# Optimization experiments

Hardware: AMD Instinct MI355X
Metric: run time of the kernel (lower is better)

The kernel has to match this reference:

```python
import jax, jax.numpy as jnp
import numpy as np

DIM = 768
NUM_HEADS = 12
HEAD_DIM = DIM // NUM_HEADS
SCALE = HEAD_DIM ** -0.5


def setup_inputs() -> dict:
    key = jax.random.key(0)
    k_x, k_qw, k_qb, k_pw, k_pb = jax.random.split(key, 5)
    B, N = 4, 2048
    x = jax.random.normal(k_x, (B, N, DIM), dtype=jnp.float32)
    s = 1.0 / np.sqrt(DIM)
    qkv_w = jax.random.normal(k_qw, (3 * DIM, DIM), dtype=jnp.float32) * s
    qkv_b = jax.random.normal(k_qb, (3 * DIM,), dtype=jnp.float32) * 0.02
    proj_w = jax.random.normal(k_pw, (DIM, DIM), dtype=jnp.float32) * s
    proj_b = jax.random.normal(k_pb, (DIM,), dtype=jnp.float32) * 0.02
    return {"x": x, "qkv_w": qkv_w, "qkv_b": qkv_b, "proj_w": proj_w, "proj_b": proj_b}


def reference(x, qkv_w, qkv_b, proj_w, proj_b):
    B, N, D = x.shape
    H, Hd = NUM_HEADS, HEAD_DIM
    # qkv linear: [B,N,3D] -> [3,B,H,N,Hd]
    qkv = (x @ qkv_w.T + qkv_b).reshape(B, N, 3, H, Hd).transpose(2, 0, 3, 1, 4)
    q, k, v = qkv[0], qkv[1], qkv[2]
    scores = jnp.einsum("bhnd,bhmd->bhnm", q, k) * SCALE  # [B,H,N,N]
    attn = jax.nn.softmax(scores, axis=-1)
    out = jnp.einsum("bhnm,bhmd->bhnd", attn, v)  # [B,H,N,Hd]
    out = out.transpose(0, 2, 1, 3).reshape(B, N, D)
    return out @ proj_w.T + proj_b
```

## Files before the change

### kernel.cpp

```cpp
#include <hip/hip_runtime.h>

#define SEQ 2048
#define NB 4
#define NH 12
#define DHEAD 64
#define DMODEL 768
#define D3 2304
#define MTOT 8192
#define QSCALE 0.18033688011112042f

typedef float f4v __attribute__((ext_vector_type(4)));
typedef float fl4 __attribute__((ext_vector_type(4)));
typedef short s8v __attribute__((ext_vector_type(8)));
typedef __bf16 b8v __attribute__((ext_vector_type(8)));
typedef unsigned int ui4 __attribute__((ext_vector_type(4)));
typedef unsigned int ui2 __attribute__((ext_vector_type(2)));
typedef unsigned short us4 __attribute__((ext_vector_type(4)));

#define GLDS16(g, l)                                                            \
  __builtin_amdgcn_global_load_lds(                                             \
      (const __attribute__((address_space(1))) void*)(g),                       \
      (__attribute__((address_space(3))) void*)(l), 16, 0, 0)

__device__ inline float fast_exp2(float x) {
#if __has_builtin(__builtin_amdgcn_exp2f)
  return __builtin_amdgcn_exp2f(x);
#else
  float r;
  asm("v_exp_f32 %0, %1" : "=v"(r) : "v"(x));
  return r;
#endif
}

template <typename T>
__device__ inline auto mfma_try(T a, T b, f4v c, int)
    -> decltype(__builtin_amdgcn_mfma_f32_16x16x32_bf16(a, b, c, 0, 0, 0)) {
  return __builtin_amdgcn_mfma_f32_16x16x32_bf16(a, b, c, 0, 0, 0);
}
template <typename T>
__device__ inline f4v mfma_try(T a, T b, f4v c, long) {
  return __builtin_amdgcn_mfma_f32_16x16x32_bf16(
      __builtin_bit_cast(b8v, a), __builtin_bit_cast(b8v, b), c, 0, 0, 0);
}
__device__ inline f4v mfma16(s8v a, s8v b, f4v c) { return mfma_try(a, b, c, 0); }

__device__ inline unsigned short f2bf(float f) {
  union { float f; unsigned u; } v; v.f = f;
  unsigned r = v.u + 0x7FFFu + ((v.u >> 16) & 1u);
  return (unsigned short)(r >> 16);
}

__device__ inline unsigned pack2(float a, float b) {
  unsigned ua = __builtin_bit_cast(unsigned, a) + 0x8000u;
  unsigned ub = __builtin_bit_cast(unsigned, b) + 0x8000u;
  return __builtin_amdgcn_perm(ub, ua, 0x07060302u);
}

#define NX4 1572864
#define NW14 442368
#define NW24 147456
__global__ void k_cvt(const float* __restrict__ x, const float* __restrict__ w1,
                      const float* __restrict__ w2, unsigned short* __restrict__ ox,
                      unsigned short* __restrict__ o1, unsigned short* __restrict__ o2) {
  int i = blockIdx.x * 256 + threadIdx.x;
  const float* src;
  unsigned short* dst;
  int off;
  if (i < NX4) { src = x; dst = ox; off = i; }
  else if (i < NX4 + NW14) { src = w1; dst = o1; off = i - NX4; }
  else if (i < NX4 + NW14 + NW24) { src = w2; dst = o2; off = i - NX4 - NW14; }
  else return;
  fl4 f = ((const fl4*)src)[off];
  us4 o;
  o[0] = f2bf(f[0]); o[1] = f2bf(f[1]); o[2] = f2bf(f[2]); o[3] = f2bf(f[3]);
  ((us4*)dst)[off] = o;
}

template <int EPI>
__global__ __launch_bounds__(256, 3) void k_gemm_nt(
    const unsigned short* __restrict__ A,
    const unsigned short* __restrict__ Bm,
    const float* __restrict__ bias,
    float* __restrict__ outF,
    unsigned short* __restrict__ outQ,
    unsigned short* __restrict__ outK,
    unsigned short* __restrict__ outV,
    int K) {
  __shared__ unsigned short As[128 * 64];
  __shared__ unsigned short Bs[128 * 64];
  const int tid = threadIdx.x;
  const int lane = tid & 63;
  const int wave = tid >> 6;
  const int wr = wave >> 1, wc = wave & 1;
  const int lr = lane & 15;
  const int lq = lane >> 4;
  const int rowBase = blockIdx.y * 128;
  const int colBase = blockIdx.x * 128;

  f4v acc[4][4];
#pragma unroll
  for (int i = 0; i < 4; ++i)
#pragma unroll
    for (int j = 0; j < 4; ++j) acc[i][j] = f4v{0.f, 0.f, 0.f, 0.f};

  const int srow = wave * 8 + (lane >> 3);
  const int scol = ((lane & 7) ^ ((lane >> 3) & 7)) * 8;
  const unsigned short* Ag0 = A + (long)(rowBase + srow) * K + scol;
  const unsigned short* Bg0 = Bm + (long)(colBase + srow) * K + scol;
  unsigned short* Al0 = &As[srow * 64 + (lane & 7) * 8];
  unsigned short* Bl0 = &Bs[srow * 64 + (lane & 7) * 8];
  const int kTiles = K >> 6;
  const int swz = (lr & 7);

  for (int kt = 0; kt < kTiles; ++kt) {
#pragma unroll
    for (int p = 0; p < 4; ++p) {
      GLDS16(Ag0 + kt * 64 + p * 32 * K, Al0 + p * 32 * 64);
      GLDS16(Bg0 + kt * 64 + p * 32 * K, Bl0 + p * 32 * 64);
    }
    __syncthreads();
#pragma unroll
    for (int ks = 0; ks < 2; ++ks) {
      s8v af[4], bf[4];
#pragma unroll
      for (int i = 0; i < 4; ++i)
        af[i] = *(const s8v*)&As[(wr * 64 + i * 16 + lr) * 64 + ((ks * 4 + lq) ^ swz) * 8];
#pragma unroll
      for (int j = 0; j < 4; ++j)
        bf[j] = *(const s8v*)&Bs[(wc * 64 + j * 16 + lr) * 64 + ((ks * 4 + lq) ^ swz) * 8];
#pragma unroll
      for (int i = 0; i < 4; ++i)
#pragma unroll
        for (int j = 0; j < 4; ++j) acc[i][j] = mfma16(af[i], bf[j], acc[i][j]);
    }
    __syncthreads();
  }

  if (EPI == 0 || EPI == 1) {
    const int fw = rowBase + wr * 64;
    fl4 bv[4];
#pragma unroll
    for (int i = 0; i < 4; ++i) bv[i] = *(const fl4*)&bias[fw + i * 16 + lq * 4];
    const int isQ = (EPI == 0) && (fw < DMODEL);
    const int h = (fw >> 6) % NH;
    const unsigned short* outQK = isQ ? outQ : outK;
    const float scl = isQ ? QSCALE : 1.0f;
#pragma unroll
    for (int j = 0; j < 4; ++j) {
      const int ng = colBase + wc * 64 + j * 16 + lr;
#pragma unroll
      for (int i = 0; i < 4; ++i) {
        float v0 = acc[i][j][0] + bv[i][0], v1 = acc[i][j][1] + bv[i][1];
        float v2 = acc[i][j][2] + bv[i][2], v3 = acc[i][j][3] + bv[i][3];
        if (EPI == 1) {
          *(fl4*)&outF[(long)ng * DMODEL + fw + i * 16 + lq * 4] = fl4{v0, v1, v2, v3};
        } else {
          const int b = ng >> 11, nn = ng & 2047;
          unsigned short* dst = (unsigned short*)outQK +
              (long)(((b * NH + h) * SEQ) + nn) * DHEAD + (i * 16 + lq * 4);
          *(ui2*)dst = ui2{pack2(v0 * scl, v1 * scl), pack2(v2 * scl, v3 * scl)};
        }
      }
    }
  } else {
#pragma unroll
    for (int j = 0; j < 4; ++j) {
      const int col = colBase + wc * 64 + j * 16 + lr;
      const float bvs = bias[col];
      const int h = col >> 6, hd = col & 63;
#pragma unroll
      for (int i = 0; i < 4; ++i) {
        const int row = rowBase + wr * 64 + i * 16 + lq * 4;
        const int b = row >> 11, n = row & 2047;
        const int bq = (n >> 2) & 7;
        const int np = (n & ~31) + ((bq & 3) << 3) + ((bq >> 2) << 2);
        float v0 = acc[i][j][0] + bvs, v1 = acc[i][j][1] + bvs;
        float v2 = acc[i][j][2] + bvs, v3 = acc[i][j][3] + bvs;
        *(ui2*)&outV[(long)(((b * NH + h) * DHEAD) + hd) * SEQ + np] =
            ui2{pack2(v0, v1), pack2(v2, v3)};
      }
    }
  }
}

__global__ __launch_bounds__(256, 3) void k_attn(
    const unsigned short* __restrict__ Q,
    const unsigned short* __restrict__ Kg,
    const unsigned short* __restrict__ Vt,
    unsigned short* __restrict__ Ob) {
  __shared__ unsigned short Ks[128 * 64];
  __shared__ unsigned short Vs[64 * 128];
  const int tid = threadIdx.x;
  const int lane = tid & 63;
  const int wave = tid >> 6;
  const int lr = lane & 15;
  const int lq = lane >> 4;
  const int bh = blockIdx.y;
  const int b = bh / NH, h = bh % NH;
  const int q0 = blockIdx.x * 128;
  const unsigned short* Qb = Q + (long)bh * SEQ * DHEAD;
  const unsigned short* Kb = Kg + (long)bh * SEQ * DHEAD;
  const unsigned short* Vb = Vt + (long)bh * DHEAD * SEQ;

  s8v qf[2][2];
#pragma unroll
  for (int i = 0; i < 2; ++i)
#pragma unroll
    for (int ss = 0; ss < 2; ++ss)
      qf[i][ss] = *(const s8v*)(Qb + (q0 + wave * 32 + i * 16 + lr) * DHEAD + ss * 32 + lq * 8);

  f4v o[2][4];
  f4v la[2] = {f4v{0.f, 0.f, 0.f, 0.f}, f4v{0.f, 0.f, 0.f, 0.f}};
  const f4v zc = f4v{0.f, 0.f, 0.f, 0.f};
  const s8v ones = {0x3F80, 0x3F80, 0x3F80, 0x3F80, 0x3F80, 0x3F80, 0x3F80, 0x3F80};
#pragma unroll
  for (int i = 0; i < 2; ++i)
#pragma unroll
    for (int jo = 0; jo < 4; ++jo) o[i][jo] = f4v{0.f, 0.f, 0.f, 0.f};

  const int srow = wave * 8 + (lane >> 3);
  const int scol = ((lane & 7) ^ ((lane >> 3) & 7)) * 8;
  const unsigned short* Kg0 = Kb + (long)srow * DHEAD + scol;
  unsigned short* Kl0 = &Ks[srow * 64 + (lane & 7) * 8];
  const int swz = (lr & 7);
  const int vdrow = wave * 4 + (lane >> 4);
  const int vchunk = (lane & 15) ^ vdrow;
  const unsigned short* Vg0 = Vb + (long)vdrow * SEQ + vchunk * 8;
  unsigned short* Vl0 = &Vs[vdrow * 128 + (lane & 15) * 8];

  for (int kt = 0; kt < SEQ / 128; ++kt) {
#pragma unroll
    for (int p = 0; p < 4; ++p)
      GLDS16(Kg0 + (long)(kt * 128 + p * 32) * DHEAD, Kl0 + p * 32 * 64);
#pragma unroll
    for (int p = 0; p < 4; ++p)
      GLDS16(Vg0 + (long)(p * 16) * SEQ + kt * 128, Vl0 + p * 16 * 128);
    __syncthreads();

    f4v s[2][8];
#pragma unroll
    for (int t = 0; t < 8; ++t) {
      s8v kf0 = *(const s8v*)&Ks[(t * 16 + lr) * 64 + ((0 * 4 + lq) ^ swz) * 8];
      s8v kf1 = *(const s8v*)&Ks[(t * 16 + lr) * 64 + ((1 * 4 + lq) ^ swz) * 8];
      s[0][t] = mfma16(kf0, qf[0][0], zc);
      s[1][t] = mfma16(kf0, qf[1][0], zc);
      s[0][t] = mfma16(kf1, qf[0][1], s[0][t]);
      s[1][t] = mfma16(kf1, qf[1][1], s[1][t]);
    }

    unsigned pk[2][8][2];
#pragma unroll
    for (int i = 0; i < 2; ++i)
#pragma unroll
      for (int t = 0; t < 8; ++t) {
        float p0 = fast_exp2(s[i][t][0]);
        float p1 = fast_exp2(s[i][t][1]);
        float p2 = fast_exp2(s[i][t][2]);
        float p3 = fast_exp2(s[i][t][3]);
        pk[i][t][0] = pack2(p0, p1);
        pk[i][t][1] = pack2(p2, p3);
      }

#pragma unroll
    for (int ss = 0; ss < 4; ++ss) {
      s8v vf[4];
#pragma unroll
      for (int jo = 0; jo < 4; ++jo)
        vf[jo] = *(const s8v*)&Vs[(jo * 16 + lr) * 128 + ((ss * 4 + lq) ^ lr) * 8];
#pragma unroll
      for (int i = 0; i < 2; ++i) {
        s8v pf = __builtin_bit_cast(
            s8v, ui4{pk[i][2 * ss][0], pk[i][2 * ss][1], pk[i][2 * ss + 1][0], pk[i][2 * ss + 1][1]});
        la[i] = mfma16(ones, pf, la[i]);
#pragma unroll
        for (int jo = 0; jo < 4; ++jo) o[i][jo] = mfma16(vf[jo], pf, o[i][jo]);
      }
    }
    __syncthreads();
  }

  float linv[2];
  linv[0] = 1.0f / la[0][0];
  linv[1] = 1.0f / la[1][0];

#pragma unroll
  for (int i = 0; i < 2; ++i) {
    const long nrow = (long)(b * SEQ + q0 + wave * 32 + i * 16 + lr) * DMODEL;
#pragma unroll
    for (int jo = 0; jo < 4; ++jo) {
      float v0 = o[i][jo][0] * linv[i];
      float v1 = o[i][jo][1] * linv[i];
      float v2 = o[i][jo][2] * linv[i];
      float v3 = o[i][jo][3] * linv[i];
      *(ui2*)(Ob + nrow + h * DHEAD + jo * 16 + lq * 4) = ui2{pack2(v0, v1), pack2(v2, v3)};
    }
  }
}

extern "C" void kernel_launch(void* const* d_in, const int* in_sizes, int n_in,
                              void* d_out, int out_size, void* d_ws, size_t ws_size,
                              hipStream_t stream) {
  (void)in_sizes; (void)n_in; (void)out_size; (void)ws_size;
  const float* x = (const float*)d_in[0];
  const float* qkv_w = (const float*)d_in[1];
  const float* qkv_b = (const float*)d_in[2];
  const float* proj_w = (const float*)d_in[3];
  const float* proj_b = (const float*)d_in[4];
  float* out = (float*)d_out;

  unsigned short* ws = (unsigned short*)d_ws;
  unsigned short* xb = ws;
  unsigned short* wqkvb = xb + 6291456;
  unsigned short* wprjb = wqkvb + 1769472;
  unsigned short* qb = wprjb + 589824;
  unsigned short* kb = qb + 6291456;
  unsigned short* vtb = kb + 6291456;
  unsigned short* aob = vtb + 6291456;

  k_cvt<<<(NX4 + NW14 + NW24 + 255) / 256, 256, 0, stream>>>(
      x, qkv_w, proj_w, xb, wqkvb, wprjb);

  k_gemm_nt<0><<<dim3(MTOT / 128, 2 * DMODEL / 128), 256, 0, stream>>>(
      wqkvb, xb, qkv_b, nullptr, qb, kb, nullptr, DMODEL);
  k_gemm_nt<2><<<dim3(DMODEL / 128, MTOT / 128), 256, 0, stream>>>(
      xb, wqkvb + 2 * DMODEL * DMODEL, qkv_b + 2 * DMODEL, nullptr, nullptr, nullptr, vtb,
      DMODEL);
  k_attn<<<dim3(SEQ / 128, NB * NH), 256, 0, stream>>>(qb, kb, vtb, aob);
  k_gemm_nt<1><<<dim3(MTOT / 128, DMODEL / 128), 256, 0, stream>>>(
      wprjb, aob, proj_b, out, nullptr, nullptr, nullptr, DMODEL);
}
```

Baseline: 207.1 us.

## Merge Q/K and V GEMMs into one launch and shrink tiles for V and proj

Q/K and V projection GEMMs are fused into a single launch, where block index selects either a 128x128 Q/K tile or a 128x64 V tile. The V and output-projection GEMMs now use 128x64 tiles, so they launch more blocks. This is meant to remove one kernel launch gap and improve wave fill for the smaller GEMMs. In exchange, the narrower tiles reuse less data from shared memory per block.

```diff
diff --git a/kernel.cpp b/kernel.cpp
--- a/kernel.cpp
+++ b/kernel.cpp
@@ -76,97 +76,128 @@
   ((us4*)dst)[off] = o;
 }
 
-template <int EPI>
-__global__ __launch_bounds__(256, 3) void k_gemm_nt(
-    const unsigned short* __restrict__ A,
-    const unsigned short* __restrict__ Bm,
-    const float* __restrict__ bias,
-    float* __restrict__ outF,
+__global__ __launch_bounds__(256, 3) void k_qkv(
+    const unsigned short* __restrict__ xb,
+    const unsigned short* __restrict__ wb,
+    const float* __restrict__ qkv_b,
     unsigned short* __restrict__ outQ,
     unsigned short* __restrict__ outK,
-    unsigned short* __restrict__ outV,
-    int K) {
+    unsigned short* __restrict__ outV) {
   __shared__ unsigned short As[128 * 64];
   __shared__ unsigned short Bs[128 * 64];
   const int tid = threadIdx.x;
   const int lane = tid & 63;
   const int wave = tid >> 6;
   const int wr = wave >> 1, wc = wave & 1;
-  const int lr = lane & 15;
-  const int lq = lane >> 4;
-  const int rowBase = blockIdx.y * 128;
-  const int colBase = blockIdx.x * 128;
-
-  f4v acc[4][4];
-#pragma unroll
-  for (int i = 0; i < 4; ++i)
-#pragma unroll
-    for (int j = 0; j < 4; ++j) acc[i][j] = f4v{0.f, 0.f, 0.f, 0.f};
-
+  const int lr = lane & 15, lq = lane >> 4;
   const int srow = wave * 8 + (lane >> 3);
   const int scol = ((lane & 7) ^ ((lane >> 3) & 7)) * 8;
-  const unsigned short* Ag0 = A + (long)(rowBase + srow) * K + scol;
-  const unsigned short* Bg0 = Bm + (long)(colBase + srow) * K + scol;
-  unsigned short* Al0 = &As[srow * 64 + (lane & 7) * 8];
-  unsigned short* Bl0 = &Bs[srow * 64 + (lane & 7) * 8];
-  const int kTiles = K >> 6;
   const int swz = (lr & 7);
-
-  for (int kt = 0; kt < kTiles; ++kt) {
-#pragma unroll
-    for (int p = 0; p < 4; ++p) {
-      GLDS16(Ag0 + kt * 64 + p * 32 * K, Al0 + p * 32 * 64);
-      GLDS16(Bg0 + kt * 64 + p * 32 * K, Bl0 + p * 32 * 64);
-    }
-    __syncthreads();
-#pragma unroll
-    for (int ks = 0; ks < 2; ++ks) {
-      s8v af[4], bf[4];
-#pragma unroll
-      for (int i = 0; i < 4; ++i)
-        af[i] = *(const s8v*)&As[(wr * 64 + i * 16 + lr) * 64 + ((ks * 4 + lq) ^ swz) * 8];
-#pragma unroll
-      for (int j = 0; j < 4; ++j)
-        bf[j] = *(const s8v*)&Bs[(wc * 64 + j * 16 + lr) * 64 + ((ks * 4 + lq) ^ swz) * 8];
-#pragma unroll
-      for (int i = 0; i < 4; ++i)
-#pragma unroll
-        for (int j = 0; j < 4; ++j) acc[i][j] = mfma16(af[i], bf[j], acc[i][j]);
-    }
-    __syncthreads();
-  }
-
-  if (EPI == 0 || EPI == 1) {
+  const int bx = blockIdx.x;
+
+  if (bx < 768) {
+    const int rowBase = (bx >> 6) * 128;
+    const int colBase = (bx & 63) * 128;
+    f4v acc[4][4];
+#pragma unroll
+    for (int i = 0; i < 4; ++i)
+#pragma unroll
+      for (int j = 0; j < 4; ++j) acc[i][j] = f4v{0.f, 0.f, 0.f, 0.f};
+
+    const unsigned short* Ag0 = wb + (long)(rowBase + srow) * DMODEL + scol;
+    const unsigned short* Bg0 = xb + (long)(colBase + srow) * DMODEL + scol;
+    unsigned short* Al0 = &As[srow * 64 + (lane & 7) * 8];
+    unsigned short* Bl0 = &Bs[srow * 64 + (lane & 7) * 8];
+
+    for (int kt = 0; kt < DMODEL / 64; ++kt) {
+#pragma unroll
+      for (int p = 0; p < 4; ++p) {
+        GLDS16(Ag0 + kt * 64 + p * 32 * DMODEL, Al0 + p * 32 * 64);
+        GLDS16(Bg0 + kt * 64 + p * 32 * DMODEL, Bl0 + p * 32 * 64);
+      }
+      __syncthreads();
+#pragma unroll
+      for (int ks = 0; ks < 2; ++ks) {
+        s8v af[4], bf[4];
+#pragma unroll
+        for (int i = 0; i < 4; ++i)
+          af[i] = *(const s8v*)&As[(wr * 64 + i * 16 + lr) * 64 + ((ks * 4 + lq) ^ swz) * 8];
+#pragma unroll
+        for (int j = 0; j < 4; ++j)
+          bf[j] = *(const s8v*)&Bs[(wc * 64 + j * 16 + lr) * 64 + ((ks * 4 + lq) ^ swz) * 8];
+#pragma unroll
+        for (int i = 0; i < 4; ++i)
+#pragma unroll
+          for (int j = 0; j < 4; ++j) acc[i][j] = mfma16(af[i], bf[j], acc[i][j]);
+      }
+      __syncthreads();
+    }
+
     const int fw = rowBase + wr * 64;
     fl4 bv[4];
 #pragma unroll
-    for (int i = 0; i < 4; ++i) bv[i] = *(const fl4*)&bias[fw + i * 16 + lq * 4];
-    const int isQ = (EPI == 0) && (fw < DMODEL);
+    for (int i = 0; i < 4; ++i) bv[i] = *(const fl4*)&qkv_b[fw + i * 16 + lq * 4];
+    const int isQ = fw < DMODEL;
     const int h = (fw >> 6) % NH;
-    const unsigned short* outQK = isQ ? outQ : outK;
+    unsigned short* outQK = (unsigned short*)(isQ ? outQ : outK);
     const float scl = isQ ? QSCALE : 1.0f;
 #pragma unroll
     for (int j = 0; j < 4; ++j) {
       const int ng = colBase + wc * 64 + j * 16 + lr;
+      const int b = ng >> 11, nn = ng & 2047;
 #pragma unroll
       for (int i = 0; i < 4; ++i) {
-        float v0 = acc[i][j][0] + bv[i][0], v1 = acc[i][j][1] + bv[i][1];
-        float v2 = acc[i][j][2] + bv[i][2], v3 = acc[i][j][3] + bv[i][3];
-        if (EPI == 1) {
-          *(fl4*)&outF[(long)ng * DMODEL + fw + i * 16 + lq * 4] = fl4{v0, v1, v2, v3};
-        } else {
-          const int b = ng >> 11, nn = ng & 2047;
-          unsigned short* dst = (unsigned short*)outQK +
-              (long)(((b * NH + h) * SEQ) + nn) * DHEAD + (i * 16 + lq * 4);
-          *(ui2*)dst = ui2{pack2(v0 * scl, v1 * scl), pack2(v2 * scl, v3 * scl)};
-        }
+        float v0 = (acc[i][j][0] + bv[i][0]) * scl, v1 = (acc[i][j][1] + bv[i][1]) * scl;
+        float v2 = (acc[i][j][2] + bv[i][2]) * scl, v3 = (acc[i][j][3] + bv[i][3]) * scl;
+        *(ui2*)(outQK + (long)(((b * NH + h) * SEQ) + nn) * DHEAD + (i * 16 + lq * 4)) =
+            ui2{pack2(v0, v1), pack2(v2, v3)};
       }
     }
   } else {
-#pragma unroll
-    for (int j = 0; j < 4; ++j) {
-      const int col = colBase + wc * 64 + j * 16 + lr;
-      const float bvs = bias[col];
+    const int vb = bx - 768;
+    const int rowBase = (vb / 12) * 128;
+    const int colBase = (vb % 12) * 64;
+    f4v acc[4][2];
+#pragma unroll
+    for (int i = 0; i < 4; ++i)
+#pragma unroll
+      for (int j = 0; j < 2; ++j) acc[i][j] = f4v{0.f, 0.f, 0.f, 0.f};
+
+    const unsigned short* Ag0 = xb + (long)(rowBase + srow) * DMODEL + scol;
+    const unsigned short* Bg0 =
+        wb + (long)(2 * DMODEL + colBase + srow) * DMODEL + scol;
+    unsigned short* Al0 = &As[srow * 64 + (lane & 7) * 8];
+    unsigned short* Bl0 = &Bs[srow * 64 + (lane & 7) * 8];
+
+    for (int kt = 0; kt < DMODEL / 64; ++kt) {
+#pragma unroll
+      for (int p = 0; p < 4; ++p)
+        GLDS16(Ag0 + kt * 64 + p * 32 * DMODEL, Al0 + p * 32 * 64);
+#pragma unroll
+      for (int p = 0; p < 2; ++p)
+        GLDS16(Bg0 + kt * 64 + p * 32 * DMODEL, Bl0 + p * 32 * 64);
+      __syncthreads();
+#pragma unroll
+      for (int ks = 0; ks < 2; ++ks) {
+        s8v af[4], bf[2];
+#pragma unroll
+        for (int i = 0; i < 4; ++i)
+          af[i] = *(const s8v*)&As[(wr * 64 + i * 16 + lr) * 64 + ((ks * 4 + lq) ^ swz) * 8];
+#pragma unroll
+        for (int j = 0; j < 2; ++j)
+          bf[j] = *(const s8v*)&Bs[(wc * 32 + j * 16 + lr) * 64 + ((ks * 4 + lq) ^ swz) * 8];
+#pragma unroll
+        for (int i = 0; i < 4; ++i)
+#pragma unroll
+          for (int j = 0; j < 2; ++j) acc[i][j] = mfma16(af[i], bf[j], acc[i][j]);
+      }
+      __syncthreads();
+    }
+
+#pragma unroll
+    for (int j = 0; j < 2; ++j) {
+      const int col = colBase + wc * 32 + j * 16 + lr;
+      const float bvs = qkv_b[2 * DMODEL + col];
       const int h = col >> 6, hd = col & 63;
 #pragma unroll
       for (int i = 0; i < 4; ++i) {
@@ -179,6 +210,76 @@
         *(ui2*)&outV[(long)(((b * NH + h) * DHEAD) + hd) * SEQ + np] =
             ui2{pack2(v0, v1), pack2(v2, v3)};
       }
+    }
+  }
+}
+
+__global__ __launch_bounds__(256, 3) void k_proj(
+    const unsigned short* __restrict__ Wp,
+    const unsigned short* __restrict__ Xt,
+    const float* __restrict__ bias,
+    float* __restrict__ outF) {
+  __shared__ unsigned short As[128 * 64];
+  __shared__ unsigned short Bs[64 * 64];
+  const int tid = threadIdx.x;
+  const int lane = tid & 63;
+  const int wave = tid >> 6;
+  const int wr = wave >> 1, wc = wave & 1;
+  const int lr = lane & 15, lq = lane >> 4;
+  const int srow = wave * 8 + (lane >> 3);
+  const int scol = ((lane & 7) ^ ((lane >> 3) & 7)) * 8;
+  const int swz = (lr & 7);
+  const int rowBase = blockIdx.y * 128;
+  const int colBase = blockIdx.x * 64;
+
+  f4v acc[4][2];
+#pragma unroll
+  for (int i = 0; i < 4; ++i)
+#pragma unroll
+    for (int j = 0; j < 2; ++j) acc[i][j] = f4v{0.f, 0.f, 0.f, 0.f};
+
+  const unsigned short* Ag0 = Wp + (long)(rowBase + srow) * DMODEL + scol;
+  const unsigned short* Bg0 = Xt + (long)(colBase + srow) * DMODEL + scol;
+  unsigned short* Al0 = &As[srow * 64 + (lane & 7) * 8];
+  unsigned short* Bl0 = &Bs[srow * 64 + (lane & 7) * 8];
+
+  for (int kt = 0; kt < DMODEL / 64; ++kt) {
+#pragma unroll
+    for (int p = 0; p < 4; ++p)
+      GLDS16(Ag0 + kt * 64 + p * 32 * DMODEL, Al0 + p * 32 * 64);
+#pragma unroll
+    for (int p = 0; p < 2; ++p)
+      GLDS16(Bg0 + kt * 64 + p * 32 * DMODEL, Bl0 + p * 32 * 64);
+    __syncthreads();
+#pragma unroll
+    for (int ks = 0; ks < 2; ++ks) {
+      s8v af[4], bf[2];
+#pragma unroll
+      for (int i = 0; i < 4; ++i)
+        af[i] = *(const s8v*)&As[(wr * 64 + i * 16 + lr) * 64 + ((ks * 4 + lq) ^ swz) * 8];
+#pragma unroll
+      for (int j = 0; j < 2; ++j)
+        bf[j] = *(const s8v*)&Bs[(wc * 32 + j * 16 + lr) * 64 + ((ks * 4 + lq) ^ swz) * 8];
+#pragma unroll
+      for (int i = 0; i < 4; ++i)
+#pragma unroll
+        for (int j = 0; j < 2; ++j) acc[i][j] = mfma16(af[i], bf[j], acc[i][j]);
+    }
+    __syncthreads();
+  }
+
+  const int fw = rowBase + wr * 64;
+  fl4 bv[4];
+#pragma unroll
+  for (int i = 0; i < 4; ++i) bv[i] = *(const fl4*)&bias[fw + i * 16 + lq * 4];
+#pragma unroll
+  for (int j = 0; j < 2; ++j) {
+    const int ng = colBase + wc * 32 + j * 16 + lr;
+#pragma unroll
+    for (int i = 0; i < 4; ++i) {
+      float v0 = acc[i][j][0] + bv[i][0], v1 = acc[i][j][1] + bv[i][1];
+      float v2 = acc[i][j][2] + bv[i][2], v3 = acc[i][j][3] + bv[i][3];
+      *(fl4*)&outF[(long)ng * DMODEL + fw + i * 16 + lq * 4] = fl4{v0, v1, v2, v3};
     }
   }
 }
@@ -320,12 +421,7 @@
   k_cvt<<<(NX4 + NW14 + NW24 + 255) / 256, 256, 0, stream>>>(
       x, qkv_w, proj_w, xb, wqkvb, wprjb);
 
-  k_gemm_nt<0><<<dim3(MTOT / 128, 2 * DMODEL / 128), 256, 0, stream>>>(
-      wqkvb, xb, qkv_b, nullptr, qb, kb, nullptr, DMODEL);
-  k_gemm_nt<2><<<dim3(DMODEL / 128, MTOT / 128), 256, 0, stream>>>(
-      xb, wqkvb + 2 * DMODEL * DMODEL, qkv_b + 2 * DMODEL, nullptr, nullptr, nullptr, vtb,
-      DMODEL);
+  k_qkv<<<1536, 256, 0, stream>>>(xb, wqkvb, qkv_b, qb, kb, vtb);
   k_attn<<<dim3(SEQ / 128, NB * NH), 256, 0, stream>>>(qb, kb, vtb, aob);
-  k_gemm_nt<1><<<dim3(MTOT / 128, DMODEL / 128), 256, 0, stream>>>(
-      wprjb, aob, proj_b, out, nullptr, nullptr, nullptr, DMODEL);
-}
+  k_proj<<<dim3(MTOT / 64, DMODEL / 128), 256, 0, stream>>>(wprjb, aob, proj_b, out);
+}
```

Measured after the change: 202.6 us. 2.2% less time.
